# Kernel tuning notes

Hardware: AMD Instinct MI355X
Metric: run time of the kernel (lower is better)

The kernel has to match this reference:

```python
import jax, jax.numpy as jnp
import numpy as np

FP8_MAX = 448.0   # max finite value of float8_e4m3fn
GROUP = 128       # quant group size (both act cols and weight blocks)


def fp8_roundtrip(v):
    # Round-to-nearest onto the fp8 e4m3fn grid, back to f32.
    return v.astype(jnp.float8_e4m3fn).astype(jnp.float32)


def setup_inputs() -> dict:
    key = jax.random.key(0)
    k1, k2, k3 = jax.random.split(key, 3)
    M, H = 8192, 4096
    x = jax.random.normal(k1, (M, 2 * H), dtype=jnp.float32)
    # weight: rand -> fp8 grid (stored as f32 values lying exactly on fp8 grid)
    w_q = fp8_roundtrip(jax.random.uniform(k2, (H, H), dtype=jnp.float32))
    # per-(128,128)-block weight scales
    wscale = jax.random.uniform(k3, (H // GROUP, H // GROUP), dtype=jnp.float32)
    return {"x": x, "w_q": w_q, "wscale": wscale}


def reference(x, w_q, wscale):
    H = x.shape[-1] // 2
    # SiluAndMul: silu(gate) * up
    y = jax.nn.silu(x[:, :H]) * x[:, H:]            # [M, H]
    M = y.shape[0]
    # --- activation group quant, group shape (1, 128) ---
    g = y.reshape(M, H // GROUP, GROUP)
    amax = jnp.max(jnp.abs(g), axis=-1, keepdims=True)
    scale = jnp.maximum(amax, 1e-12) / FP8_MAX      # [M, H/128, 1]
    q = fp8_roundtrip(g / scale)                    # fp8-grid values
    y_dq = (q * scale).reshape(M, H)                # dequantized activation
    # --- weight block dequant, block shape (128, 128) ---
    nk, nn = H // GROUP, H // GROUP
    w_dq = (w_q.reshape(nk, GROUP, nn, GROUP) * wscale[:, None, :, None]).reshape(H, H)
    # block-fp8 linear: out[m, n] = sum_k y_dq[m, k] * w_dq[k, n]
    return y_dq @ w_dq
```

## Files before the change

### kernel.cpp

```cpp
#include <hip/hip_runtime.h>
#include <hip/hip_fp8.h>
#include <hip/hip_bf16.h>

#define MDIM 8192
#define HDIM 4096
#define NKT 64

typedef float f32x4 __attribute__((ext_vector_type(4)));
typedef short bf16x8 __attribute__((ext_vector_type(8)));
typedef unsigned short u16x4 __attribute__((ext_vector_type(4)));

__device__ inline void gload_lds16(const void* g, void* l) {
  __builtin_amdgcn_global_load_lds(
      (const __attribute__((address_space(1))) void*)g,
      (__attribute__((address_space(3))) void*)l, 16, 0, 0);
}

__device__ inline unsigned short f2bf(float f) {
  __hip_bfloat16 h = __float2bfloat16(f);
  return *reinterpret_cast<unsigned short*>(&h);
}

__global__ __launch_bounds__(256) void silu_quant_kernel(
    const float* __restrict__ x, unsigned short* __restrict__ yb) {
  const int m = blockIdx.x;
  const int t = threadIdx.x;
  const int g = t >> 3;
  const int i = t & 7;
  const float* xr = x + (size_t)m * (2 * HDIM);

  float v[16];
  float amax = 0.f;
#pragma unroll
  for (int j = 0; j < 4; ++j) {
    const int off = g * 128 + j * 32 + i * 4;
    f32x4 gate = *(const f32x4*)(xr + off);
    f32x4 up = *(const f32x4*)(xr + HDIM + off);
#pragma unroll
    for (int c = 0; c < 4; ++c) {
      float gg = gate[c];
      float s = gg / (1.f + expf(-gg));
      float val = s * up[c];
      v[j * 4 + c] = val;
      amax = fmaxf(amax, fabsf(val));
    }
  }
#pragma unroll
  for (int d = 1; d < 8; d <<= 1) amax = fmaxf(amax, __shfl_xor(amax, d, 64));
  const float scale = fmaxf(amax, 1e-12f) / 448.0f;

#pragma unroll
  for (int j = 0; j < 4; ++j) {
    u16x4 pk;
#pragma unroll
    for (int c = 0; c < 4; ++c) {
      __hip_fp8_e4m3 qv(v[j * 4 + c] / scale);
      pk[c] = f2bf((float)qv * scale);
    }
    *(u16x4*)(yb + (size_t)m * HDIM + g * 128 + j * 32 + i * 4) = pk;
  }
}

__global__ __launch_bounds__(256) void wconv_kernel(
    const float* __restrict__ w, const float* __restrict__ wsc,
    unsigned short* __restrict__ wt) {
  __shared__ unsigned short tile[64][66];
  const int t = threadIdx.x;
  const int n0 = (blockIdx.x & 63) * 64;
  const int k0 = (blockIdx.x >> 6) * 64;
  const float ws = wsc[(k0 >> 7) * 32 + (n0 >> 7)];
  {
    const int r = t >> 4;
    const int c4 = (t & 15) << 2;
#pragma unroll
    for (int j = 0; j < 4; ++j) {
      const int kr = r + j * 16;
      f32x4 vv = *(const f32x4*)(w + (size_t)(k0 + kr) * HDIM + n0 + c4);
#pragma unroll
      for (int c = 0; c < 4; ++c) tile[kr][c4 + c] = f2bf(vv[c] * ws);
    }
  }
  __syncthreads();
  {
    const int n = t >> 4;
    const int k4 = (t & 15) << 2;
#pragma unroll
    for (int j = 0; j < 4; ++j) {
      const int nn = n + j * 16;
      u16x4 pk;
#pragma unroll
      for (int c = 0; c < 4; ++c) pk[c] = tile[k4 + c][nn];
      *(u16x4*)(wt + (size_t)(n0 + nn) * HDIM + k0 + k4) = pk;
    }
  }
}

#define SCHED0 __builtin_amdgcn_sched_barrier(0)
#define SBAR do { SCHED0; __builtin_amdgcn_s_barrier(); SCHED0; } while (0)
#define VMW0 asm volatile("s_waitcnt vmcnt(0)" ::: "memory")
#define LGKM0 asm volatile("s_waitcnt lgkmcnt(0)" ::: "memory")
#define PRIO1 __builtin_amdgcn_s_setprio(1)
#define PRIO0 __builtin_amdgcn_s_setprio(0)

#define STAGE_UNIT(bi, kt, u) do {                                          \
    const __hip_bfloat16* gsrc;  unsigned char* ldst;                       \
    if ((u) == 0)      { gsrc = A + (size_t)(m0 + r0) * HDIM;       ldst = As[bi]; }          \
    else if ((u) == 1) { gsrc = B + (size_t)(n0 + r0) * HDIM;       ldst = Bs[bi]; }          \
    else if ((u) == 2) { gsrc = A + (size_t)(m0 + 128 + r0) * HDIM; ldst = As[bi] + 16384; }  \
    else               { gsrc = B + (size_t)(n0 + 128 + r0) * HDIM; ldst = Bs[bi] + 16384; }  \
    gsrc += (size_t)(kt) * 64 + cst * 8;                                    \
    gload_lds16(gsrc, ldst + t * 16);                                       \
    gload_lds16(gsrc + (size_t)64 * HDIM, ldst + 8192 + t * 16);            \
  } while (0)

#define RD_A(c, mh, dst) do { _Pragma("unroll") for (int mi = 0; mi < 4; ++mi) { \
    const int row = wm * 128 + (mh) * 64 + mi * 16 + lrow;                       \
    _Pragma("unroll") for (int kk = 0; kk < 2; ++kk)                             \
      dst[mi][kk] = *(const bf16x8*)(As[c] + row * 128 + (((kk * 4 + lhi) ^ rx) * 16)); \
  } } while (0)

#define RD_B(c, nh, dst) do { _Pragma("unroll") for (int ni = 0; ni < 2; ++ni) { \
    const int row = wn * 64 + (nh) * 32 + ni * 16 + lrow;                        \
    _Pragma("unroll") for (int kk = 0; kk < 2; ++kk)                             \
      dst[ni][kk] = *(const bf16x8*)(Bs[c] + row * 128 + (((kk * 4 + lhi) ^ rx) * 16)); \
  } } while (0)

#define MFMA16(AF, BF, MB, NB) do { _Pragma("unroll") for (int kk = 0; kk < 2; ++kk) \
    _Pragma("unroll") for (int mi = 0; mi < 4; ++mi)                                 \
      _Pragma("unroll") for (int ni = 0; ni < 2; ++ni)                               \
        acc[(MB) + mi][(NB) + ni] = __builtin_amdgcn_mfma_f32_16x16x32_bf16(         \
            AF[mi][kk], BF[ni][kk], acc[(MB) + mi][(NB) + ni], 0, 0, 0);             \
  } while (0)

#define ITER(j, SH) do {                                                     \
    const int c_ = (j) & 1, n_ = c_ ^ 1;                                     \
                          \
    RD_A(c_, 0, afr0); RD_B(c_, 0, bfr0);                                    \
    if (SH) { STAGE_UNIT(n_, (j) + 1, 0); STAGE_UNIT(n_, (j) + 1, 1); }      \
    SBAR; LGKM0; SCHED0;                                                     \
    PRIO1; MFMA16(afr0, bfr0, 0, 0); PRIO0;                                  \
    SBAR;                                                                    \
                          \
    RD_A(c_, 1, afr1);                                                       \
    if (SH) { STAGE_UNIT(n_, (j) + 1, 2); STAGE_UNIT(n_, (j) + 1, 3); }      \
    SBAR; LGKM0; SCHED0;                                                     \
    PRIO1; MFMA16(afr1, bfr0, 4, 0); PRIO0;                                  \
    SBAR;                                                                    \
                                                     \
    RD_B(c_, 1, bfr1);                                                       \
    SBAR; LGKM0; SCHED0;                                                     \
    PRIO1; MFMA16(afr1, bfr1, 4, 2); PRIO0;                                  \
    SBAR;                                                                    \
       \
    PRIO1; MFMA16(afr0, bfr1, 0, 2); PRIO0;                                  \
    SCHED0; VMW0; SBAR;                                                      \
  } while (0)

__global__ __launch_bounds__(512, 1) void gemm_bf16_kernel(
    const __hip_bfloat16* __restrict__ A,
    const __hip_bfloat16* __restrict__ B,
    float* __restrict__ out) {
  __shared__ __align__(16) unsigned char As[2][32768];
  __shared__ __align__(16) unsigned char Bs[2][32768];

  const int bid = blockIdx.x;
  const int x = bid & 7, sub = bid >> 3;
  const int mtile = (x >> 1) * 8 + (sub & 7);
  const int ntile = (x & 1) * 8 + (sub >> 3);
  const int m0 = mtile * 256, n0 = ntile * 256;

  const int t = threadIdx.x;
  const int l = t & 63, wid = t >> 6;
  const int wm = wid >> 2, wn = wid & 3;
  const int lrow = l & 15, lhi = l >> 4;
  const int rx = lrow & 7;

  const int r0 = t >> 3;
  const int cst = (t & 7) ^ (r0 & 7);

  f32x4 acc[8][4];
#pragma unroll
  for (int a = 0; a < 8; ++a)
#pragma unroll
    for (int b = 0; b < 4; ++b) acc[a][b] = (f32x4){0.f, 0.f, 0.f, 0.f};
  bf16x8 afr0[4][2], afr1[4][2], bfr0[2][2], bfr1[2][2];

  STAGE_UNIT(0, 0, 0); STAGE_UNIT(0, 0, 1); STAGE_UNIT(0, 0, 2); STAGE_UNIT(0, 0, 3);
  VMW0;
  SBAR;

  for (int j = 0; j < NKT - 1; ++j) ITER(j, 1);
  ITER(NKT - 1, 0);

#pragma unroll
  for (int mi = 0; mi < 8; ++mi)
#pragma unroll
    for (int r = 0; r < 4; ++r) {
      const int grow = m0 + wm * 128 + mi * 16 + lhi * 4 + r;
      float* orow = out + (size_t)grow * HDIM + n0 + wn * 64 + lrow;
#pragma unroll
      for (int ni = 0; ni < 4; ++ni) orow[ni * 16] = acc[mi][ni][r];
    }
}

extern "C" void kernel_launch(void* const* d_in, const int* in_sizes, int n_in,
                              void* d_out, int out_size, void* d_ws, size_t ws_size,
                              hipStream_t stream) {
  const float* x = (const float*)d_in[0];
  const float* wq = (const float*)d_in[1];
  const float* wsc = (const float*)d_in[2];
  float* out = (float*)d_out;

  unsigned short* yb = (unsigned short*)d_ws;
  unsigned short* wt = yb + (size_t)MDIM * HDIM;

  silu_quant_kernel<<<MDIM, 256, 0, stream>>>(x, yb);
  wconv_kernel<<<(HDIM / 64) * (HDIM / 64), 256, 0, stream>>>(wq, wsc, wt);
  gemm_bf16_kernel<<<(MDIM / 256) * (HDIM / 256), 512, 0, stream>>>(
      (const __hip_bfloat16*)yb, (const __hip_bfloat16*)wt, out);
}
```

Before: 330.3 us.

## Deepen GEMM global-to-LDS prefetch pipeline across two k-tiles

Restructures the bf16 GEMM main loop to process two k-tiles per iteration and issue LDS staging loads further ahead, about 1.75 tiles of lookahead, while reusing the same double buffer. Loads for a buffer are issued as soon as its fragments have been read, and partial vmcnt waits replace full drains, so global memory latency overlaps more of the MFMA work. This adds complexity and risks correctness hazards, because staging writes into a buffer while other waves may still be reading it, guarded only by the barriers placed between phases.

```diff
diff --git a/kernel.cpp b/kernel.cpp
--- a/kernel.cpp
+++ b/kernel.cpp
@@ -97,7 +97,7 @@
 
 #define SCHED0 __builtin_amdgcn_sched_barrier(0)
 #define SBAR do { SCHED0; __builtin_amdgcn_s_barrier(); SCHED0; } while (0)
-#define VMW0 asm volatile("s_waitcnt vmcnt(0)" ::: "memory")
+#define VMW(n) asm volatile("s_waitcnt vmcnt(" #n ")" ::: "memory")
 #define LGKM0 asm volatile("s_waitcnt lgkmcnt(0)" ::: "memory")
 #define PRIO1 __builtin_amdgcn_s_setprio(1)
 #define PRIO0 __builtin_amdgcn_s_setprio(0)
@@ -132,28 +132,53 @@
             AF[mi][kk], BF[ni][kk], acc[(MB) + mi][(NB) + ni], 0, 0, 0);             \
   } while (0)
 
-#define ITER(j, SH) do {                                                     \
-    const int c_ = (j) & 1, n_ = c_ ^ 1;                                     \
-                          \
-    RD_A(c_, 0, afr0); RD_B(c_, 0, bfr0);                                    \
-    if (SH) { STAGE_UNIT(n_, (j) + 1, 0); STAGE_UNIT(n_, (j) + 1, 1); }      \
+#define ITER2(kt2, SHM, VM4, VM8) do {                                       \
+                                 \
+    RD_A(0, 0, afr0); RD_B(0, 0, bfr0);                                      \
+    STAGE_UNIT(1, (kt2) + 1, 3);                                             \
     SBAR; LGKM0; SCHED0;                                                     \
     PRIO1; MFMA16(afr0, bfr0, 0, 0); PRIO0;                                  \
     SBAR;                                                                    \
-                          \
-    RD_A(c_, 1, afr1);                                                       \
-    if (SH) { STAGE_UNIT(n_, (j) + 1, 2); STAGE_UNIT(n_, (j) + 1, 3); }      \
+                                          \
+    RD_A(0, 1, afr1);                                                        \
+    if (SHM) STAGE_UNIT(0, (kt2) + 2, 0);                                    \
     SBAR; LGKM0; SCHED0;                                                     \
     PRIO1; MFMA16(afr1, bfr0, 4, 0); PRIO0;                                  \
     SBAR;                                                                    \
-                                                     \
-    RD_B(c_, 1, bfr1);                                                       \
+                                          \
+    RD_B(0, 1, bfr1);                                                        \
+    if (SHM) STAGE_UNIT(0, (kt2) + 2, 1);                                    \
     SBAR; LGKM0; SCHED0;                                                     \
     PRIO1; MFMA16(afr1, bfr1, 4, 2); PRIO0;                                  \
     SBAR;                                                                    \
-       \
+      \
+    if (SHM) STAGE_UNIT(0, (kt2) + 2, 2);                                    \
+    SBAR;                                                                    \
     PRIO1; MFMA16(afr0, bfr1, 0, 2); PRIO0;                                  \
-    SCHED0; VMW0; SBAR;                                                      \
+    VM4; SBAR;                                                               \
+                               \
+    RD_A(1, 0, afr0); RD_B(1, 0, bfr0);                                      \
+    if (SHM) STAGE_UNIT(0, (kt2) + 2, 3);                                    \
+    SBAR; LGKM0; SCHED0;                                                     \
+    PRIO1; MFMA16(afr0, bfr0, 0, 0); PRIO0;                                  \
+    SBAR;                                                                    \
+                                          \
+    RD_A(1, 1, afr1);                                                        \
+    if (SHM) STAGE_UNIT(1, (kt2) + 3, 0);                                    \
+    SBAR; LGKM0; SCHED0;                                                     \
+    PRIO1; MFMA16(afr1, bfr0, 4, 0); PRIO0;                                  \
+    SBAR;                                                                    \
+                                          \
+    RD_B(1, 1, bfr1);                                                        \
+    if (SHM) STAGE_UNIT(1, (kt2) + 3, 1);                                    \
+    SBAR; LGKM0; SCHED0;                                                     \
+    PRIO1; MFMA16(afr1, bfr1, 4, 2); PRIO0;                                  \
+    SBAR;                                                                    \
+                \
+    if (SHM) STAGE_UNIT(1, (kt2) + 3, 2);                                    \
+    SBAR;                                                                    \
+    PRIO1; MFMA16(afr0, bfr1, 0, 2); PRIO0;                                  \
+    VM8; SBAR;                                                               \
   } while (0)
 
 __global__ __launch_bounds__(512, 1) void gemm_bf16_kernel(
@@ -186,11 +211,12 @@
   bf16x8 afr0[4][2], afr1[4][2], bfr0[2][2], bfr1[2][2];
 
   STAGE_UNIT(0, 0, 0); STAGE_UNIT(0, 0, 1); STAGE_UNIT(0, 0, 2); STAGE_UNIT(0, 0, 3);
-  VMW0;
+  STAGE_UNIT(1, 1, 0); STAGE_UNIT(1, 1, 1); STAGE_UNIT(1, 1, 2);
+  VMW(6);
   SBAR;
 
-  for (int j = 0; j < NKT - 1; ++j) ITER(j, 1);
-  ITER(NKT - 1, 0);
+  for (int kt2 = 0; kt2 < NKT - 2; kt2 += 2) ITER2(kt2, 1, VMW(6), VMW(6));
+  ITER2(NKT - 2, 0, VMW(0), (void)0);
 
 #pragma unroll
   for (int mi = 0; mi < 8; ++mi)
```

New measurement: 324.4 us. Within noise of the previous version (-1.8%).
